# Optimization experiments

Measured on AMD Instinct MI355X. Metric: run time of the kernel, lower is better.

The kernel has to match this reference:

```python
import jax, jax.numpy as jnp
import numpy as np

B, S, D, H, DFF = 8, 1024, 1024, 16, 4096
HD = D // H
EPS_COS = 1e-8
EPS_LN = 1e-5


def setup_inputs() -> dict:
    key = jax.random.key(0)
    ks = jax.random.split(key, 12)
    inp = {
        "x": jax.random.normal(ks[0], (B, S, D), jnp.float32),
        "ln1_w": jnp.ones((D,), jnp.float32),
        "ln1_b": jnp.zeros((D,), jnp.float32),
        "in_proj_w": jax.random.normal(ks[1], (3 * D, D), jnp.float32) * 0.02,
        "in_proj_b": jnp.zeros((3 * D,), jnp.float32),
        "out_proj_w": jax.random.normal(ks[2], (D, D), jnp.float32) * 0.02,
        "out_proj_b": jnp.zeros((D,), jnp.float32),
        "ln2_w": jnp.ones((D,), jnp.float32),
        "ln2_b": jnp.zeros((D,), jnp.float32),
        "mu_weight": jax.random.uniform(ks[3], (DFF, D), jnp.float32, -1.0, 1.0) * (1.0 / np.sqrt(D)),
        "sigma_weight": jax.random.normal(ks[4], (DFF, D), jnp.float32) * 0.02,
        "gate_param": jnp.full((DFF,), 0.1, jnp.float32),
        "mu_bias": jnp.zeros((DFF,), jnp.float32),
        "ffn2_w": jax.random.normal(ks[5], (D, DFF), jnp.float32) * 0.02,
        "ffn2_b": jnp.zeros((D,), jnp.float32),
    }
    return inp


def _layernorm(x, w, b):
    mu = jnp.mean(x, axis=-1, keepdims=True)
    var = jnp.mean(jnp.square(x - mu), axis=-1, keepdims=True)
    return (x - mu) * jax.lax.rsqrt(var + EPS_LN) * w + b


def _mha_causal(h, in_proj_w, in_proj_b, out_proj_w, out_proj_b):
    # h: [B,S,D]; combined qkv projection as in torch nn.MultiheadAttention
    qkv = h @ in_proj_w.T + in_proj_b                      # [B,S,3D]
    q, k, v = jnp.split(qkv, 3, axis=-1)
    def heads(t):
        return t.reshape(B, S, H, HD).transpose(0, 2, 1, 3)  # [B,H,S,HD]
    q, k, v = heads(q), heads(k), heads(v)
    logits = jnp.einsum("bhqd,bhkd->bhqk", q, k) / jnp.sqrt(jnp.float32(HD))
    causal = jnp.tril(jnp.ones((S, S), bool))
    logits = jnp.where(causal, logits, jnp.float32(-jnp.inf))
    attn = jax.nn.softmax(logits, axis=-1)
    o = jnp.einsum("bhqk,bhkd->bhqd", attn, v)
    o = o.transpose(0, 2, 1, 3).reshape(B, S, D)
    return o @ out_proj_w.T + out_proj_b


def _moie_linear(xr, mu_weight, sigma_weight, gate_param, mu_bias):
    # xr: [N,D]. cosine similarity via GEMM + norm reductions (no (N,out,in) blowup)
    keys = mu_weight * jax.nn.softplus(sigma_weight)       # [DFF,D]
    dots = xr @ keys.T                                      # [N,DFF]
    xn = jnp.maximum(jnp.linalg.norm(xr, axis=-1, keepdims=True), EPS_COS)
    kn = jnp.maximum(jnp.linalg.norm(keys, axis=-1), EPS_COS)
    scores = dots / (xn * kn[None, :])                      # [N,DFF]
    weights = jax.nn.relu(scores - gate_param[None, :])
    comp = xr @ mu_weight.T + mu_bias                       # [N,DFF]
    masked = comp * weights
    return masked, scores


def reference(x, ln1_w, ln1_b, in_proj_w, in_proj_b, out_proj_w, out_proj_b,
              ln2_w, ln2_b, mu_weight, sigma_weight, gate_param, mu_bias,
              ffn2_w, ffn2_b):
    h = _layernorm(x, ln1_w, ln1_b)
    attn_out = _mha_causal(h, in_proj_w, in_proj_b, out_proj_w, out_proj_b)
    x = x + attn_out
    ffn_in = _layernorm(x, ln2_w, ln2_b)
    xr = ffn_in.reshape(-1, D)                              # [N,D]
    masked, scores = _moie_linear(xr, mu_weight, sigma_weight, gate_param, mu_bias)
    ffn1_out = masked.reshape(B, S, DFF)
    act = jax.nn.silu(ffn1_out)
    ffn2_out = act @ ffn2_w.T + ffn2_b
    x = x + ffn2_out
    return x, scores, masked
```

## Files before the change

### kernel.cpp

```cpp
#include <hip/hip_runtime.h>

typedef unsigned short u16;
typedef unsigned int u32;
typedef unsigned long long u64;
typedef __attribute__((ext_vector_type(8))) short short8;
typedef __attribute__((ext_vector_type(4))) float f32x4;

#define DEV static __device__ __forceinline__

DEV u16 f2b(float f) {
  union { float f; u32 u; } a; a.f = f;
  u32 r = a.u + 0x7fffu + ((a.u >> 16) & 1u);
  return (u16)(r >> 16);
}

DEV f32x4 mfma16(short8 a, short8 b, f32x4 c) {
  return __builtin_amdgcn_mfma_f32_16x16x32_bf16(a, b, c, 0, 0, 0);
}

DEV void async16(const void* g, void* l) {
  __builtin_amdgcn_global_load_lds(
      (const __attribute__((address_space(1))) u32*)g,
      (__attribute__((address_space(3))) u32*)l, 16, 0, 0);
}

__global__ __launch_bounds__(256) void f2bf4(const float* __restrict__ src,
                                             u16* __restrict__ dst, int n4) {
  const int stride = gridDim.x * 256;
  for (int i = blockIdx.x * 256 + threadIdx.x; i < n4; i += stride) {
    const f32x4 v = ((const f32x4*)src)[i];
    union { u64 q; u16 s[4]; } pk;
    pk.s[0] = f2b(v[0]); pk.s[1] = f2b(v[1]); pk.s[2] = f2b(v[2]); pk.s[3] = f2b(v[3]);
    ((u64*)dst)[i] = pk.q;
  }
}

__global__ __launch_bounds__(256) void prep_keys(
    const float* __restrict__ mu, const float* __restrict__ sg,
    u16* __restrict__ wcat, float* __restrict__ kn) {
  __shared__ float s1[4];
  const int row = blockIdx.x, tid = threadIdx.x, lane = tid & 63, wave = tid >> 6;
  const f32x4 m = *(const f32x4*)(mu + (size_t)row * 1024 + tid * 4);
  const f32x4 s = *(const f32x4*)(sg + (size_t)row * 1024 + tid * 4);
  float q = 0.f;
  union { u64 q; u16 s[4]; } pkk, pkm;
  #pragma unroll
  for (int j = 0; j < 4; ++j) {
    const float sp = (s[j] > 20.f) ? s[j] : log1pf(__expf(s[j]));
    const float k = m[j] * sp;
    q += k * k;
    pkk.s[j] = f2b(k);
    pkm.s[j] = f2b(m[j]);
  }
  *(u64*)(wcat + (size_t)row * 1024 + tid * 4) = pkk.q;
  *(u64*)(wcat + (size_t)(4096 + row) * 1024 + tid * 4) = pkm.q;
  #pragma unroll
  for (int d = 1; d < 64; d <<= 1) q += __shfl_xor(q, d);
  if (lane == 0) s1[wave] = q;
  __syncthreads();
  if (tid == 0) kn[row] = 1.0f / fmaxf(sqrtf(s1[0] + s1[1] + s1[2] + s1[3]), 1e-8f);
}

__global__ __launch_bounds__(256) void ln_kernel(
    const float* __restrict__ x, const float* __restrict__ w,
    const float* __restrict__ b, u16* __restrict__ y, float* __restrict__ xn) {
  __shared__ float s1[4], s2[4];
  const int row = blockIdx.x, tid = threadIdx.x, lane = tid & 63, wave = tid >> 6;
  const f32x4 xv = *(const f32x4*)(x + (size_t)row * 1024 + tid * 4);
  float s = xv[0] + xv[1] + xv[2] + xv[3];
  float q = xv[0]*xv[0] + xv[1]*xv[1] + xv[2]*xv[2] + xv[3]*xv[3];
  #pragma unroll
  for (int d = 1; d < 64; d <<= 1) { s += __shfl_xor(s, d); q += __shfl_xor(q, d); }
  if (lane == 0) { s1[wave] = s; s2[wave] = q; }
  __syncthreads();
  s = s1[0] + s1[1] + s1[2] + s1[3];
  q = s2[0] + s2[1] + s2[2] + s2[3];
  const float mean = s * (1.f / 1024.f);
  const float inv = rsqrtf(q * (1.f / 1024.f) - mean * mean + 1e-5f);
  const f32x4 wv = *(const f32x4*)(w + tid * 4);
  const f32x4 bv = *(const f32x4*)(b + tid * 4);
  float yv[4];
  union { u64 q; u16 s[4]; } pk;
  #pragma unroll
  for (int j = 0; j < 4; ++j) {
    yv[j] = (xv[j] - mean) * inv * wv[j] + bv[j];
    pk.s[j] = f2b(yv[j]);
  }
  *(u64*)(y + (size_t)row * 1024 + tid * 4) = pk.q;
  if (xn) {
    float qs = yv[0]*yv[0] + yv[1]*yv[1] + yv[2]*yv[2] + yv[3]*yv[3];
    #pragma unroll
    for (int d = 1; d < 64; d <<= 1) qs += __shfl_xor(qs, d);
    __syncthreads();
    if (lane == 0) s1[wave] = qs;
    __syncthreads();
    if (tid == 0) xn[row] = 1.0f / fmaxf(sqrtf(s1[0] + s1[1] + s1[2] + s1[3]), 1e-8f);
  }
}

template<int MODE, int BM>
__global__ __launch_bounds__(512, 2) void gemm_bt(
    const u16* __restrict__ A, const u16* __restrict__ W,
    int M, int N, int K,
    const float* __restrict__ aux0, const float* __restrict__ aux1,
    float* __restrict__ fo0,
    u16* __restrict__ bo0, u16* __restrict__ bo1, u16* __restrict__ bo2) {
  constexpr int MF = BM / 32;
  constexpr int A_U16 = BM * 32;
  constexpr int STRIDE = A_U16 + 8192;
  constexpr int AISS = BM / 128;
  constexpr int LPT = AISS + 2;
  __shared__ __align__(16) u16 lds[3 * STRIDE];

  const int tid = threadIdx.x;
  const int lane = tid & 63, wave = tid >> 6;
  const int x = lane & 15, g = lane >> 4;
  const int wm = wave >> 2, wn = wave & 3;

  const int gx = N >> 8;
  const int nwg = gridDim.x;
  const int wg = ((int)blockIdx.x & 7) * (nwg >> 3) + ((int)blockIdx.x >> 3);
  const int by = wg / gx, bx = wg - by * gx;
  const int m0 = by * BM, n0 = bx * 256;

  const u16* srcA[AISS]; const u16* srcB[2];
  int dA[AISS], dB[2];
  #pragma unroll
  for (int i = 0; i < AISS; ++i) {
    const int rp = i * 64 + (tid >> 3);
    const int pre = (tid & 7) ^ (rp & 7);
    const int row = rp * 2 + (pre & 1), col = (pre >> 1) * 8;
    srcA[i] = A + (size_t)(m0 + row) * K + col;
    dA[i] = i * 4096 + tid * 8;
  }
  #pragma unroll
  for (int i = 0; i < 2; ++i) {
    const int rp = i * 64 + (tid >> 3);
    const int pre = (tid & 7) ^ (rp & 7);
    const int row = rp * 2 + (pre & 1), col = (pre >> 1) * 8;
    srcB[i] = W + (size_t)(n0 + row) * K + col;
    dB[i] = A_U16 + i * 4096 + tid * 8;
  }
  const int lane_off = (x >> 1) * 64 + (((2 * g + (x & 1)) ^ (x >> 1)) * 8);
  const int aoff = wm * (BM / 4) * 64 + lane_off;
  const int boff = A_U16 + wn * 2048 + lane_off;

  f32x4 acc[MF][4];
  #pragma unroll
  for (int f = 0; f < MF; ++f)
    #pragma unroll
    for (int j = 0; j < 4; ++j) acc[f][j] = (f32x4){0.f, 0.f, 0.f, 0.f};

  const int NT = K >> 5;
  auto stage = [&](int t, int b) {
    u16* buf = lds + b * STRIDE;
    const size_t ko = (size_t)t * 32;
    #pragma unroll
    for (int i = 0; i < AISS; ++i) async16(srcA[i] + ko, buf + dA[i]);
    #pragma unroll
    for (int i = 0; i < 2; ++i) async16(srcB[i] + ko, buf + dB[i]);
  };
  stage(0, 0);
  stage(1, 1);
  int br = 0, bs = 2;
  for (int t = 0; t < NT; ++t) {
    if (t < NT - 1)
      asm volatile("s_waitcnt vmcnt(%0)\n\ts_barrier" :: "n"(LPT) : "memory");
    else
      asm volatile("s_waitcnt vmcnt(0)\n\ts_barrier" ::: "memory");
    const u16* bufr = lds + br * STRIDE;
    short8 bfr[4], af[MF];
    #pragma unroll
    for (int j = 0; j < 4; ++j) bfr[j] = *(const short8*)(bufr + boff + j * 512);
    #pragma unroll
    for (int f = 0; f < MF; ++f) af[f] = *(const short8*)(bufr + aoff + f * 512);
    if (t + 2 < NT) stage(t + 2, bs);
    __builtin_amdgcn_s_setprio(1);
    #pragma unroll
    for (int f = 0; f < MF; ++f)
      #pragma unroll
      for (int j = 0; j < 4; ++j) acc[f][j] = mfma16(af[f], bfr[j], acc[f][j]);
    __builtin_amdgcn_s_setprio(0);
    br = (br == 2) ? 0 : br + 1;
    bs = (bs == 2) ? 0 : bs + 1;
  }

  const int col_base = n0 + wn * 64;
  const int row_base = m0 + wm * (BM / 2);
  #pragma unroll
  for (int f = 0; f < MF; ++f)
    #pragma unroll
    for (int j = 0; j < 4; ++j)
      #pragma unroll
      for (int r = 0; r < 4; ++r) {
        const int row = row_base + f * 16 + g * 4 + r;
        const int col = col_base + j * 16 + x;
        float v = acc[f][j][r];
        if constexpr (MODE == 0) {
          v += aux0[col];
          const int part = col >> 10, cc = col & 1023;
          const int hh = cc >> 6, dd = cc & 63;
          const size_t idx = ((size_t)((row >> 10) * 16 + hh) * 1024 + (row & 1023)) * 64 + dd;
          if (part == 0) bo0[idx] = f2b(v * 0.125f);
          else if (part == 1) bo1[idx] = f2b(v);
          else bo2[idx] = f2b(v);
        } else if constexpr (MODE == 1) {
          fo0[(size_t)row * 1024 + col] = v + aux0[col] + aux1[(size_t)row * 1024 + col];
        } else {
          __builtin_nontemporal_store(
              v + aux0[col] + aux1[(size_t)row * 1024 + col],
              &fo0[(size_t)row * 1024 + col]);
        }
      }
}

__global__ __launch_bounds__(512, 2) void moie_gemm(
    const u16* __restrict__ A, const u16* __restrict__ W,
    const float* __restrict__ xni, const float* __restrict__ kni,
    const float* __restrict__ mub, const float* __restrict__ gate,
    float* __restrict__ oscore, float* __restrict__ omask,
    u16* __restrict__ oact) {
  __shared__ __align__(16) u16 lds[4 * 16384];
  const int tid = threadIdx.x;
  const int lane = tid & 63, wave = tid >> 6;
  const int x = lane & 15, g = lane >> 4, h = x >> 1, pp = x & 1;
  const int wm = wave >> 2, wn = wave & 3;

  const int bid = (int)blockIdx.x;
  const int local = bid >> 3;
  const int by = (bid & 7) * 4 + (local & 3);
  const int bx = local >> 2;
  const int m0 = by * 256, n0 = bx * 128;

  const int rp0 = tid >> 3, j0 = tid & 7;
  const int prow = rp0 * 2 + (j0 & 1);
  const int pcol = (((j0 >> 1) ^ (rp0 & 3)) & 3) * 8;
  const u16* Asrc[2]; const u16* Bsrc[2];
  Asrc[0] = A + (size_t)(m0 + prow) * 1024 + pcol;
  Asrc[1] = A + (size_t)(m0 + 128 + prow) * 1024 + pcol;
  #pragma unroll
  for (int c = 0; c < 2; ++c) {
    const int rb = c * 128 + prow;
    const u16* base = (rb & 32) ? (W + (size_t)4096 * 1024) : W;
    Bsrc[c] = base + (size_t)(n0 + ((rb >> 6) << 5) + (rb & 31)) * 1024 + pcol;
  }
  const int dst0 = tid * 8;
  const int laneoff = h * 64 + (((2 * g + pp) ^ ((h & 3) << 1)) * 8);

  f32x4 acc[8][4];
  #pragma unroll
  for (int i = 0; i < 8; ++i)
    #pragma unroll
    for (int j = 0; j < 4; ++j) acc[i][j] = (f32x4){0.f, 0.f, 0.f, 0.f};

  auto stageA = [&](int t) {
    u16* dst = lds + (t & 3) * 16384 + dst0;
    const int ko = t * 32;
    async16(Asrc[0] + ko, dst);
    async16(Asrc[1] + ko, dst + 4096);
  };
  auto stageB = [&](int t) {
    u16* dst = lds + (t & 3) * 16384 + 8192 + dst0;
    const int ko = t * 32;
    async16(Bsrc[0] + ko, dst);
    async16(Bsrc[1] + ko, dst + 4096);
  };

  stageA(0); stageB(0); stageA(1); stageB(1); stageA(2); stageB(2);
  asm volatile("s_waitcnt vmcnt(8)\n\ts_barrier" ::: "memory");

  constexpr int NT = 32;
  for (int t = 0; t < NT; ++t) {
    const u16* bufA = lds + (t & 3) * 16384;
    const u16* bufB = bufA + 8192;
    short8 bf[4], af[8];
    #pragma unroll
    for (int j = 0; j < 4; ++j)
      bf[j] = *(const short8*)(bufB + wn * 2048 + j * 512 + laneoff);
    #pragma unroll
    for (int f = 0; f < 8; ++f)
      af[f] = *(const short8*)(bufA + wm * 4096 + f * 512 + laneoff);
    if (t + 3 < NT) { stageB(t + 3); stageA(t + 3); }
    __builtin_amdgcn_s_setprio(1);
    #pragma unroll
    for (int f = 0; f < 8; ++f)
      #pragma unroll
      for (int j = 0; j < 4; ++j) acc[f][j] = mfma16(af[f], bf[j], acc[f][j]);
    __builtin_amdgcn_s_setprio(0);
    if (t <= NT - 4)
      asm volatile("s_waitcnt vmcnt(8)\n\ts_barrier" ::: "memory");
    else if (t == NT - 3)
      asm volatile("s_waitcnt vmcnt(4)\n\ts_barrier" ::: "memory");
    else if (t == NT - 2)
      asm volatile("s_waitcnt vmcnt(0)\n\ts_barrier" ::: "memory");
  }

  #pragma unroll
  for (int i = 0; i < 8; ++i) {
    const int row = m0 + wm * 128 + i * 16 + g * 4;
    const f32x4 xv = *(const f32x4*)(xni + row);
    #pragma unroll
    for (int jj = 0; jj < 2; ++jj) {
      const int gcol = n0 + wn * 32 + jj * 16 + x;
      const float kv = kni[gcol], gt = gate[gcol], mb = mub[gcol];
      #pragma unroll
      for (int r = 0; r < 4; ++r) {
        const float s = acc[i][jj][r] * xv[r] * kv;
        const float comp = acc[i][jj + 2][r] + mb;
        const float mk = comp * fmaxf(s - gt, 0.f);
        oscore[(size_t)(row + r) * 4096 + gcol] = s;
        omask[(size_t)(row + r) * 4096 + gcol] = mk;
        oact[(size_t)(row + r) * 4096 + gcol] = f2b(mk / (1.f + __expf(-mk)));
      }
    }
  }
}

__global__ __launch_bounds__(256) void attn_kernel(
    const u16* __restrict__ Q, const u16* __restrict__ Kg,
    const u16* __restrict__ Vg, u16* __restrict__ O) {
  __shared__ __align__(16) u16 Kl[64 * 72];
  __shared__ __align__(16) u16 Vt[64 * 72];
  __shared__ __align__(16) u16 Pl[4][16 * 72];
  const int bh = blockIdx.x;
  const int qt = blockIdx.y;
  const int tid = threadIdx.x, lane = tid & 63, wave = tid >> 6;
  const int x = lane & 15, g = lane >> 4;
  const u16* Qb = Q + (size_t)bh * 1024 * 64;
  const u16* Kb = Kg + (size_t)bh * 1024 * 64;
  const u16* Vb = Vg + (size_t)bh * 1024 * 64;
  const int qbase = qt * 64 + wave * 16;
  const short8 qf0 = *(const short8*)&Qb[(qbase + x) * 64 + g * 8];
  const short8 qf1 = *(const short8*)&Qb[(qbase + x) * 64 + 32 + g * 8];
  float mrun[4], lrun[4];
  f32x4 oacc[4];
  #pragma unroll
  for (int r = 0; r < 4; ++r) { mrun[r] = -1e30f; lrun[r] = 0.f; }
  #pragma unroll
  for (int d = 0; d < 4; ++d) oacc[d] = (f32x4){0.f, 0.f, 0.f, 0.f};

  for (int t = 0; t <= qt; ++t) {
    __syncthreads();
    #pragma unroll
    for (int p = 0; p < 2; ++p) {
      const int s = tid + p * 256;
      const int row = s >> 3, c = s & 7;
      *(short8*)&Kl[row * 72 + c * 8] = *(const short8*)&Kb[(size_t)(t * 64 + row) * 64 + c * 8];
    }
    #pragma unroll
    for (int p = 0; p < 2; ++p) {
      const int kv = (tid >> 3) + p * 32;
      const int d0 = (tid & 7) * 8;
      const short8 v8 = *(const short8*)&Vb[(size_t)(t * 64 + kv) * 64 + d0];
      #pragma unroll
      for (int j = 0; j < 8; ++j) {
        const int d = d0 + j;
        Vt[d * 72 + ((kv + 8 * ((d >> 3) & 7)) & 63)] = (u16)v8[j];
      }
    }
    __syncthreads();

    float sc[4][4];
    #pragma unroll
    for (int nb = 0; nb < 4; ++nb) {
      f32x4 a = (f32x4){0.f, 0.f, 0.f, 0.f};
      const short8 kf0 = *(const short8*)&Kl[(nb * 16 + x) * 72 + g * 8];
      const short8 kf1 = *(const short8*)&Kl[(nb * 16 + x) * 72 + 32 + g * 8];
      a = mfma16(qf0, kf0, a);
      a = mfma16(qf1, kf1, a);
      #pragma unroll
      for (int r = 0; r < 4; ++r) sc[nb][r] = a[r];
    }
    if (t == qt) {
      #pragma unroll
      for (int nb = 0; nb < 4; ++nb)
        #pragma unroll
        for (int r = 0; r < 4; ++r)
          if (t * 64 + nb * 16 + x > qbase + g * 4 + r) sc[nb][r] = -1e30f;
    }
    float mnew[4], psum[4], scl[4];
    #pragma unroll
    for (int r = 0; r < 4; ++r) {
      float mx = fmaxf(fmaxf(sc[0][r], sc[1][r]), fmaxf(sc[2][r], sc[3][r]));
      #pragma unroll
      for (int d = 1; d < 16; d <<= 1) mx = fmaxf(mx, __shfl_xor(mx, d));
      mnew[r] = fmaxf(mrun[r], mx);
      scl[r] = __expf(mrun[r] - mnew[r]);
      mrun[r] = mnew[r];
      psum[r] = 0.f;
    }
    float p[4][4];
    #pragma unroll
    for (int nb = 0; nb < 4; ++nb)
      #pragma unroll
      for (int r = 0; r < 4; ++r) {
        p[nb][r] = __expf(sc[nb][r] - mnew[r]);
        psum[r] += p[nb][r];
      }
    #pragma unroll
    for (int r = 0; r < 4; ++r) {
      #pragma unroll
      for (int d = 1; d < 16; d <<= 1) psum[r] += __shfl_xor(psum[r], d);
      lrun[r] = lrun[r] * scl[r] + psum[r];
      #pragma unroll
      for (int db = 0; db < 4; ++db) oacc[db][r] *= scl[r];
    }
    u16* Pw = Pl[wave];
    #pragma unroll
    for (int nb = 0; nb < 4; ++nb)
      #pragma unroll
      for (int r = 0; r < 4; ++r)
        Pw[(g * 4 + r) * 72 + nb * 16 + x] = f2b(p[nb][r]);
    const short8 pf0 = *(const short8*)&Pw[x * 72 + g * 8];
    const short8 pf1 = *(const short8*)&Pw[x * 72 + 32 + g * 8];
    #pragma unroll
    for (int db = 0; db < 4; ++db) {
      const int d = db * 16 + x;
      const int swz = 8 * ((d >> 3) & 7);
      const short8 vf0 = *(const short8*)&Vt[d * 72 + ((g * 8 + swz) & 63)];
      const short8 vf1 = *(const short8*)&Vt[d * 72 + ((g * 8 + 32 + swz) & 63)];
      oacc[db] = mfma16(pf0, vf0, oacc[db]);
      oacc[db] = mfma16(pf1, vf1, oacc[db]);
    }
  }
  const int b = bh >> 4, hh = bh & 15;
  #pragma unroll
  for (int db = 0; db < 4; ++db)
    #pragma unroll
    for (int r = 0; r < 4; ++r) {
      const int qrow = qbase + g * 4 + r;
      O[((size_t)(b * 1024 + qrow)) * 1024 + hh * 64 + db * 16 + x] = f2b(oacc[db][r] / lrun[r]);
    }
}

extern "C" void kernel_launch(void* const* d_in, const int* in_sizes, int n_in,
                              void* d_out, int out_size, void* d_ws, size_t ws_size,
                              hipStream_t stream) {
  const float* x    = (const float*)d_in[0];
  const float* ln1w = (const float*)d_in[1];
  const float* ln1b = (const float*)d_in[2];
  const float* wip  = (const float*)d_in[3];
  const float* bip  = (const float*)d_in[4];
  const float* wop  = (const float*)d_in[5];
  const float* bop  = (const float*)d_in[6];
  const float* ln2w = (const float*)d_in[7];
  const float* ln2b = (const float*)d_in[8];
  const float* muw  = (const float*)d_in[9];
  const float* sgw  = (const float*)d_in[10];
  const float* gate = (const float*)d_in[11];
  const float* mub  = (const float*)d_in[12];
  const float* wf2  = (const float*)d_in[13];
  const float* bf2  = (const float*)d_in[14];

  float* out_x = (float*)d_out;
  float* out_scores = out_x + (size_t)8192 * 1024;
  float* out_masked = out_scores + (size_t)8192 * 4096;

  char* ws = (char*)d_ws;
  size_t off = 0;
  auto alloc = [&](size_t n) { char* p = ws + off; off += (n + 255) & ~(size_t)255; return p; };
  u16* h_bf    = (u16*)alloc((size_t)8192 * 1024 * 2);
  u16* q_bf    = (u16*)alloc((size_t)8192 * 1024 * 2);
  u16* k_bf    = (u16*)alloc((size_t)8192 * 1024 * 2);
  u16* v_bf    = (u16*)alloc((size_t)8192 * 1024 * 2);
  u16* o_bf    = (u16*)alloc((size_t)8192 * 1024 * 2);
  float* x_res = (float*)alloc((size_t)8192 * 1024 * 4);
  u16* xr_bf   = (u16*)alloc((size_t)8192 * 1024 * 2);
  float* xn    = (float*)alloc((size_t)8192 * 4);
  float* kn    = (float*)alloc((size_t)4096 * 4);
  u16* wcat    = (u16*)alloc((size_t)8192 * 1024 * 2);
  u16* wip_b   = (u16*)alloc((size_t)3072 * 1024 * 2);
  u16* wop_b   = (u16*)alloc((size_t)1024 * 1024 * 2);
  u16* wf2_b   = (u16*)alloc((size_t)1024 * 4096 * 2);
  u16* act_bf  = (u16*)alloc((size_t)8192 * 4096 * 2);

  f2bf4<<<1024, 256, 0, stream>>>(wip, wip_b, 3072 * 1024 / 4);
  f2bf4<<<512, 256, 0, stream>>>(wop, wop_b, 1024 * 1024 / 4);
  f2bf4<<<1024, 256, 0, stream>>>(wf2, wf2_b, 1024 * 4096 / 4);
  prep_keys<<<4096, 256, 0, stream>>>(muw, sgw, wcat, kn);
  ln_kernel<<<8192, 256, 0, stream>>>(x, ln1w, ln1b, h_bf, nullptr);
  gemm_bt<0, 128><<<768, 512, 0, stream>>>(h_bf, wip_b, 8192, 3072, 1024,
      bip, nullptr, nullptr, q_bf, k_bf, v_bf);
  attn_kernel<<<dim3(128, 16), 256, 0, stream>>>(q_bf, k_bf, v_bf, o_bf);
  gemm_bt<1, 128><<<256, 512, 0, stream>>>(o_bf, wop_b, 8192, 1024, 1024,
      bop, x, x_res, nullptr, nullptr, nullptr);
  ln_kernel<<<8192, 256, 0, stream>>>(x_res, ln2w, ln2b, xr_bf, xn);
  moie_gemm<<<1024, 512, 0, stream>>>(xr_bf, wcat, xn, kn, mub, gate,
      out_scores, out_masked, act_bf);
  gemm_bt<3, 128><<<256, 512, 0, stream>>>(act_bf, wf2_b, 8192, 1024, 4096,
      bf2, x_res, out_x, nullptr, nullptr, nullptr);
}
```

Measured before the change: 527.5 us.

## Pre-transpose V and double-buffer K/V tiles with async LDS loads in attention

Adds a separate kernel that transposes V into a per-head [d, seq] layout. The attention kernel then stages K and V^T tiles through double-buffered LDS using direct global-to-LDS async loads with an XOR swizzle, which replaces the synchronous register-staged loads and the scalar transpose scatter. This lets loading the next tile overlap with compute on the current one and removes one barrier per iteration. The cost is an extra kernel launch plus a full read and write of V, and a larger LDS footprint that may lower occupancy.

Result: no change. 517.5 us (-1.9%).

```diff
diff --git a/kernel.cpp b/kernel.cpp
--- a/kernel.cpp
+++ b/kernel.cpp
@@ -316,22 +316,53 @@
   }
 }
 
+__global__ __launch_bounds__(256) void vtrans(const u16* __restrict__ v,
+                                              u16* __restrict__ vt) {
+  __shared__ u16 tl[64 * 66];
+  const int bh = blockIdx.y, s0 = blockIdx.x * 64;
+  const int tid = threadIdx.x;
+  const int r8 = tid >> 3, c8 = tid & 7;
+  #pragma unroll
+  for (int p = 0; p < 2; ++p) {
+    const int row = r8 + p * 32;
+    *(short8*)&tl[row * 66 + c8 * 8] =
+        *(const short8*)&v[((size_t)bh * 1024 + s0 + row) * 64 + c8 * 8];
+  }
+  __syncthreads();
+  #pragma unroll
+  for (int p = 0; p < 2; ++p) {
+    const int d = r8 + p * 32;
+    union { short8 v; u16 s[8]; } pk;
+    #pragma unroll
+    for (int j = 0; j < 8; ++j) pk.s[j] = tl[(c8 * 8 + j) * 66 + d];
+    *(short8*)&vt[((size_t)bh * 64 + d) * 1024 + s0 + c8 * 8] = pk.v;
+  }
+}
+
 __global__ __launch_bounds__(256) void attn_kernel(
     const u16* __restrict__ Q, const u16* __restrict__ Kg,
-    const u16* __restrict__ Vg, u16* __restrict__ O) {
-  __shared__ __align__(16) u16 Kl[64 * 72];
-  __shared__ __align__(16) u16 Vt[64 * 72];
-  __shared__ __align__(16) u16 Pl[4][16 * 72];
+    const u16* __restrict__ Vtg, u16* __restrict__ O) {
+  __shared__ __align__(16) u16 Kb[2][4096];
+  __shared__ __align__(16) u16 Vb[2][4096];
+  __shared__ __align__(16) u16 Pl[4][1024];
   const int bh = blockIdx.x;
   const int qt = blockIdx.y;
   const int tid = threadIdx.x, lane = tid & 63, wave = tid >> 6;
   const int x = lane & 15, g = lane >> 4;
   const u16* Qb = Q + (size_t)bh * 1024 * 64;
-  const u16* Kb = Kg + (size_t)bh * 1024 * 64;
-  const u16* Vb = Vg + (size_t)bh * 1024 * 64;
   const int qbase = qt * 64 + wave * 16;
   const short8 qf0 = *(const short8*)&Qb[(qbase + x) * 64 + g * 8];
   const short8 qf1 = *(const short8*)&Qb[(qbase + x) * 64 + 32 + g * 8];
+
+  const int rp = tid >> 3, j0 = tid & 7;
+  const int prow = rp * 2 + (j0 & 1);
+  const int pcol = (((j0 >> 1) ^ (rp & 3)) & 3) * 8;
+  const u16* srcK = Kg + (size_t)bh * 65536 + (size_t)prow * 64 + pcol;
+  const u16* srcV = Vtg + (size_t)(bh * 64 + prow) * 1024 + pcol;
+  const int dst0 = tid * 8;
+  const int h = x >> 1, pq = x & 1;
+  const int laneoff = h * 64 + (((2 * g + pq) ^ ((h & 3) << 1)) * 8);
+
   float mrun[4], lrun[4];
   f32x4 oacc[4];
   #pragma unroll
@@ -339,33 +370,28 @@
   #pragma unroll
   for (int d = 0; d < 4; ++d) oacc[d] = (f32x4){0.f, 0.f, 0.f, 0.f};
 
+  auto stage = [&](int t) {
+    u16* kd = Kb[t & 1] + dst0;
+    u16* vd = Vb[t & 1] + dst0;
+    const u16* ks = srcK + t * 4096;
+    const u16* vs = srcV + t * 64;
+    async16(ks, kd);        async16(ks + 32, kd + 2048);
+    async16(vs, vd);        async16(vs + 32, vd + 2048);
+  };
+  stage(0);
+  asm volatile("s_waitcnt vmcnt(0)\n\ts_barrier" ::: "memory");
+
   for (int t = 0; t <= qt; ++t) {
-    __syncthreads();
-    #pragma unroll
-    for (int p = 0; p < 2; ++p) {
-      const int s = tid + p * 256;
-      const int row = s >> 3, c = s & 7;
-      *(short8*)&Kl[row * 72 + c * 8] = *(const short8*)&Kb[(size_t)(t * 64 + row) * 64 + c * 8];
-    }
-    #pragma unroll
-    for (int p = 0; p < 2; ++p) {
-      const int kv = (tid >> 3) + p * 32;
-      const int d0 = (tid & 7) * 8;
-      const short8 v8 = *(const short8*)&Vb[(size_t)(t * 64 + kv) * 64 + d0];
-      #pragma unroll
-      for (int j = 0; j < 8; ++j) {
-        const int d = d0 + j;
-        Vt[d * 72 + ((kv + 8 * ((d >> 3) & 7)) & 63)] = (u16)v8[j];
-      }
-    }
-    __syncthreads();
+    const u16* kb = Kb[t & 1];
+    const u16* vb = Vb[t & 1];
+    if (t < qt) stage(t + 1);
 
     float sc[4][4];
     #pragma unroll
     for (int nb = 0; nb < 4; ++nb) {
       f32x4 a = (f32x4){0.f, 0.f, 0.f, 0.f};
-      const short8 kf0 = *(const short8*)&Kl[(nb * 16 + x) * 72 + g * 8];
-      const short8 kf1 = *(const short8*)&Kl[(nb * 16 + x) * 72 + 32 + g * 8];
+      const short8 kf0 = *(const short8*)(kb + nb * 512 + laneoff);
+      const short8 kf1 = *(const short8*)(kb + 2048 + nb * 512 + laneoff);
       a = mfma16(qf0, kf0, a);
       a = mfma16(qf1, kf1, a);
       #pragma unroll
@@ -407,21 +433,29 @@
     }
     u16* Pw = Pl[wave];
     #pragma unroll
-    for (int nb = 0; nb < 4; ++nb)
-      #pragma unroll
-      for (int r = 0; r < 4; ++r)
-        Pw[(g * 4 + r) * 72 + nb * 16 + x] = f2b(p[nb][r]);
-    const short8 pf0 = *(const short8*)&Pw[x * 72 + g * 8];
-    const short8 pf1 = *(const short8*)&Pw[x * 72 + 32 + g * 8];
+    for (int nb = 0; nb < 4; ++nb) {
+      const int half = nb >> 1;
+      #pragma unroll
+      for (int r = 0; r < 4; ++r) {
+        const int qr = g * 4 + r;
+        const int col5 = (nb & 1) * 16 + x;
+        const int c8 = col5 >> 3, c7 = col5 & 7;
+        const int rq = qr >> 1;
+        const int jq = (qr & 1) | ((c8 ^ (rq & 3)) << 1);
+        Pw[half * 512 + rq * 64 + jq * 8 + c7] = f2b(p[nb][r]);
+      }
+    }
+    const short8 pf0 = *(const short8*)(Pw + laneoff);
+    const short8 pf1 = *(const short8*)(Pw + 512 + laneoff);
     #pragma unroll
     for (int db = 0; db < 4; ++db) {
-      const int d = db * 16 + x;
-      const int swz = 8 * ((d >> 3) & 7);
-      const short8 vf0 = *(const short8*)&Vt[d * 72 + ((g * 8 + swz) & 63)];
-      const short8 vf1 = *(const short8*)&Vt[d * 72 + ((g * 8 + 32 + swz) & 63)];
+      const short8 vf0 = *(const short8*)(vb + db * 512 + laneoff);
+      const short8 vf1 = *(const short8*)(vb + 2048 + db * 512 + laneoff);
       oacc[db] = mfma16(pf0, vf0, oacc[db]);
       oacc[db] = mfma16(pf1, vf1, oacc[db]);
     }
+    if (t < qt)
+      asm volatile("s_waitcnt vmcnt(0)\n\ts_barrier" ::: "memory");
   }
   const int b = bh >> 4, hh = bh & 15;
   #pragma unroll
@@ -463,6 +497,7 @@
   u16* q_bf    = (u16*)alloc((size_t)8192 * 1024 * 2);
   u16* k_bf    = (u16*)alloc((size_t)8192 * 1024 * 2);
   u16* v_bf    = (u16*)alloc((size_t)8192 * 1024 * 2);
+  u16* vt_bf   = (u16*)alloc((size_t)8192 * 1024 * 2);
   u16* o_bf    = (u16*)alloc((size_t)8192 * 1024 * 2);
   float* x_res = (float*)alloc((size_t)8192 * 1024 * 4);
   u16* xr_bf   = (u16*)alloc((size_t)8192 * 1024 * 2);
@@ -481,7 +516,8 @@
   ln_kernel<<<8192, 256, 0, stream>>>(x, ln1w, ln1b, h_bf, nullptr);
   gemm_bt<0, 128><<<768, 512, 0, stream>>>(h_bf, wip_b, 8192, 3072, 1024,
       bip, nullptr, nullptr, q_bf, k_bf, v_bf);
-  attn_kernel<<<dim3(128, 16), 256, 0, stream>>>(q_bf, k_bf, v_bf, o_bf);
+  vtrans<<<dim3(16, 128), 256, 0, stream>>>(v_bf, vt_bf);
+  attn_kernel<<<dim3(128, 16), 256, 0, stream>>>(q_bf, k_bf, vt_bf, o_bf);
   gemm_bt<1, 128><<<256, 512, 0, stream>>>(o_bf, wop_b, 8192, 1024, 1024,
       bop, x, x_res, nullptr, nullptr, nullptr);
   ln_kernel<<<8192, 256, 0, stream>>>(x_res, ln2w, ln2b, xr_bf, xn);
```
